# Kernel tuning notes

Measured on AMD Instinct MI355X. Metric: run time of the kernel, lower is better.

Reference implementation:

```python
import jax, jax.numpy as jnp
import numpy as np

B, S, D, H = 8, 1024, 768, 12
DH = D // H
EPS = 1e-5


def setup_inputs() -> dict:
    key = jax.random.key(0)
    ks = jax.random.split(key, 12)
    sc_h = 1.0 / np.sqrt(DH)
    sc_d = 1.0 / np.sqrt(D)
    return {
        "x": jax.random.normal(ks[0], (B, S, D), jnp.float32),
        "ln1_g": jnp.ones((D,), jnp.float32),
        "ln1_b": jnp.zeros((D,), jnp.float32),
        "Wq": jax.random.normal(ks[1], (H, DH, DH), jnp.float32) * sc_h,
        "bq": jax.random.normal(ks[2], (H, DH), jnp.float32) * 0.01,
        "Wk": jax.random.normal(ks[3], (H, DH, DH), jnp.float32) * sc_h,
        "bk": jax.random.normal(ks[4], (H, DH), jnp.float32) * 0.01,
        "Wv": jax.random.normal(ks[5], (H, DH, DH), jnp.float32) * sc_h,
        "bv": jax.random.normal(ks[6], (H, DH), jnp.float32) * 0.01,
        "ln2_g": jnp.ones((D,), jnp.float32),
        "ln2_b": jnp.zeros((D,), jnp.float32),
        "W1": jax.random.normal(ks[7], (D, 4 * D), jnp.float32) * sc_d,  # c_fc (bias=False)
        "W2": jax.random.normal(ks[8], (4 * D, D), jnp.float32) * (1.0 / np.sqrt(4 * D)),  # c_proj (bias=False)
    }


def _layernorm(x, g, b):
    m = jnp.mean(x, axis=-1, keepdims=True)
    v = jnp.mean(jnp.square(x - m), axis=-1, keepdims=True)
    return (x - m) * jax.lax.rsqrt(v + EPS) * g + b


def _msa(x, Wq, bq, Wk, bk, Wv, bv):
    b, s, d = x.shape
    h = x.reshape(b, s, H, DH)  # per-head slices of the embedding
    q = jnp.einsum('bshd,hde->bhse', h, Wq) + bq[None, :, None, :]
    k = jnp.einsum('bshd,hde->bhse', h, Wk) + bk[None, :, None, :]
    v = jnp.einsum('bshd,hde->bhse', h, Wv) + bv[None, :, None, :]
    scores = jnp.einsum('bhse,bhte->bhst', q, k) / np.sqrt(DH).astype(np.float32)
    attn = jax.nn.softmax(scores, axis=-1)
    o = jnp.einsum('bhst,bhte->bhse', attn, v)
    return o.transpose(0, 2, 1, 3).reshape(b, s, d)  # concat heads


def reference(x, ln1_g, ln1_b, Wq, bq, Wk, bk, Wv, bv, ln2_g, ln2_b, W1, W2):
    out = x + _msa(_layernorm(x, ln1_g, ln1_b), Wq, bq, Wk, bk, Wv, bv)
    h = _layernorm(out, ln2_g, ln2_b)
    ffn = jnp.dot(jax.nn.gelu(jnp.dot(h, W1), approximate=False), W2)
    return out + ffn
```

## Files before the change

kernel.cpp:

```cpp
#include <hip/hip_runtime.h>
#include <hip/hip_bf16.h>
#include <math.h>

#define B_ 8
#define S_ 1024
#define D_ 768
#define H_ 12
#define QSCALE 0.18033688011112042f

typedef __attribute__((ext_vector_type(8))) short short8;
typedef __attribute__((ext_vector_type(4))) float floatx4;
typedef unsigned short ushort_t;

__device__ __forceinline__ ushort_t f2bf(float f) {
  unsigned int u = __builtin_bit_cast(unsigned int, f);
  u += 0x7fffu + ((u >> 16) & 1u);
  return (ushort_t)(u >> 16);
}

__device__ __forceinline__ unsigned int pkbf(float a, float b) {
  __hip_bfloat162 h = __float22bfloat162_rn(make_float2(a, b));
  unsigned int r;
  __builtin_memcpy(&r, &h, sizeof(r));
  return r;
}

__device__ __forceinline__ float gelu_f(float x) {
  const float z = fabsf(x) * 0.70710678118654752f;
  const float t = __builtin_amdgcn_rcpf(1.0f + 0.3275911f * z);
  const float p =
      t * (0.254829592f +
           t * (-0.284496736f +
                t * (1.421413741f + t * (-1.453152027f + t * 1.061405429f))));
  const float e = __expf(-z * z);
  const float erfv = 1.0f - p * e;
  return 0.5f * x * (1.0f + copysignf(erfv, x));
}

template <int N>
__device__ __forceinline__ void wait_vmcnt() {
  if constexpr (N == 0)
    asm volatile("s_waitcnt vmcnt(0)" ::: "memory");
  else if constexpr (N == 3)
    asm volatile("s_waitcnt vmcnt(3)" ::: "memory");
  else if constexpr (N == 4)
    asm volatile("s_waitcnt vmcnt(4)" ::: "memory");
  else if constexpr (N == 6)
    asm volatile("s_waitcnt vmcnt(6)" ::: "memory");
  else
    asm volatile("s_waitcnt vmcnt(8)" ::: "memory");
}

__global__ __launch_bounds__(256) void ln_bf16(
    const float* __restrict__ in, const float* __restrict__ g,
    const float* __restrict__ bias, ushort_t* __restrict__ out) {
  const int row = blockIdx.x * 4 + (threadIdx.x >> 6);
  const int lane = threadIdx.x & 63;
  const float* p = in + (size_t)row * D_;
  float4 v[3];
#pragma unroll
  for (int j = 0; j < 3; ++j) v[j] = *(const float4*)(p + j * 256 + lane * 4);
  float s = 0.f;
#pragma unroll
  for (int j = 0; j < 3; ++j) s += (v[j].x + v[j].y) + (v[j].z + v[j].w);
#pragma unroll
  for (int m = 1; m < 64; m <<= 1) s += __shfl_xor(s, m);
  const float mean = s * (1.0f / D_);
  float q = 0.f;
#pragma unroll
  for (int j = 0; j < 3; ++j) {
    const float a = v[j].x - mean, b = v[j].y - mean;
    const float c = v[j].z - mean, d = v[j].w - mean;
    q += (a * a + b * b) + (c * c + d * d);
  }
#pragma unroll
  for (int m = 1; m < 64; m <<= 1) q += __shfl_xor(q, m);
  const float rstd = rsqrtf(q * (1.0f / D_) + 1e-5f);
  ushort_t* o = out + (size_t)row * D_;
#pragma unroll
  for (int j = 0; j < 3; ++j) {
    const float4 gv = *(const float4*)(g + j * 256 + lane * 4);
    const float4 bv = *(const float4*)(bias + j * 256 + lane * 4);
    const unsigned int p01 = pkbf((v[j].x - mean) * rstd * gv.x + bv.x,
                                  (v[j].y - mean) * rstd * gv.y + bv.y);
    const unsigned int p23 = pkbf((v[j].z - mean) * rstd * gv.z + bv.z,
                                  (v[j].w - mean) * rstd * gv.w + bv.w);
    *(uint2*)(o + j * 256 + lane * 4) = make_uint2(p01, p23);
  }
}

__device__ __forceinline__ void tcast_body(
    const float* __restrict__ W, ushort_t* __restrict__ Wt,
    int Kdim, int Ndim, int bx, int by, float* sh) {
  float(*tile)[33] = (float(*)[33])sh;
  const int n0 = bx * 32, k0 = by * 32;
  const int tx = threadIdx.x & 31, ty = threadIdx.x >> 5;
#pragma unroll
  for (int i = 0; i < 32; i += 8)
    tile[ty + i][tx] = W[(size_t)(k0 + ty + i) * Ndim + n0 + tx];
  __syncthreads();
#pragma unroll
  for (int i = 0; i < 32; i += 8)
    Wt[(size_t)(n0 + ty + i) * Kdim + k0 + tx] = f2bf(tile[tx][ty + i]);
}

__global__ __launch_bounds__(256) void prep_weights(
    const float* __restrict__ W1, ushort_t* __restrict__ Wt1,
    const float* __restrict__ W2, ushort_t* __restrict__ Wt2,
    const float* __restrict__ Wq, const float* __restrict__ Wk,
    const float* __restrict__ Wv, ushort_t* __restrict__ Wqt,
    ushort_t* __restrict__ Wkt, ushort_t* __restrict__ Wvt) {
  __shared__ float sh[64 * 65];
  const int bid = blockIdx.x;
  if (bid < 2304) {
    tcast_body(W1, Wt1, 768, 3072, bid % 96, bid / 96, sh);
  } else if (bid < 4608) {
    const int idx = bid - 2304;
    tcast_body(W2, Wt2, 3072, 768, idx % 24, idx / 24, sh);
  } else {
    const int idx = bid - 4608;
    const int h = idx % 12, which = idx / 12;
    const float* W = which == 0 ? Wq : which == 1 ? Wk : Wv;
    ushort_t* O = which == 0 ? Wqt : which == 1 ? Wkt : Wvt;
    float(*t)[65] = (float(*)[65])sh;
    const int tid = threadIdx.x;
#pragma unroll
    for (int i = 0; i < 16; ++i) {
      const int idx2 = tid + i * 256;
      t[idx2 >> 6][idx2 & 63] = W[h * 4096 + idx2];
    }
    __syncthreads();
#pragma unroll
    for (int i = 0; i < 16; ++i) {
      const int idx2 = tid + i * 256;
      O[h * 4096 + idx2] = f2bf(t[idx2 & 63][idx2 >> 6]);
    }
  }
}

__global__ __launch_bounds__(256) void qkv_mfma(
    const ushort_t* __restrict__ xbf,
    const ushort_t* __restrict__ Wqt, const ushort_t* __restrict__ Wkt,
    const ushort_t* __restrict__ Wvt,
    const float* __restrict__ bq, const float* __restrict__ bk,
    const float* __restrict__ bv,
    ushort_t* __restrict__ qo, ushort_t* __restrict__ ko,
    ushort_t* __restrict__ vt) {
  const int h = blockIdx.y;
  const int mb = blockIdx.x * 128;
  const int tid = threadIdx.x;
  const int wave = tid >> 6, lane = tid & 63;
  const int lc = lane & 15, kq = lane >> 4;
  const int wm = wave * 32;

  __shared__ __align__(16) ushort_t Lb[4][2560];
  ushort_t* Lw = Lb[wave];

  short8 af[2][2];
#pragma unroll
  for (int mi = 0; mi < 2; ++mi)
#pragma unroll
    for (int kc = 0; kc < 2; ++kc)
      af[mi][kc] = *(const short8*)(xbf + (size_t)(mb + wm + mi * 16 + lc) * D_ +
                                    h * 64 + kc * 32 + kq * 8);

  const ushort_t* Wp[3] = {Wqt + h * 4096, Wkt + h * 4096, Wvt + h * 4096};
  floatx4 accT[2][2][4] = {};
  floatx4 accV[2][4] = {};
#pragma unroll
  for (int n = 0; n < 4; ++n)
#pragma unroll
    for (int kc = 0; kc < 2; ++kc) {
      const short8 wq_ = *(const short8*)(Wp[0] + (n * 16 + lc) * 64 +
                                          kc * 32 + kq * 8);
      const short8 wk_ = *(const short8*)(Wp[1] + (n * 16 + lc) * 64 +
                                          kc * 32 + kq * 8);
      const short8 wv_ = *(const short8*)(Wp[2] + (n * 16 + lc) * 64 +
                                          kc * 32 + kq * 8);
#pragma unroll
      for (int mi = 0; mi < 2; ++mi) {
        accT[0][mi][n] = __builtin_amdgcn_mfma_f32_16x16x32_bf16(
            wq_, af[mi][kc], accT[0][mi][n], 0, 0, 0);
        accT[1][mi][n] = __builtin_amdgcn_mfma_f32_16x16x32_bf16(
            wk_, af[mi][kc], accT[1][mi][n], 0, 0, 0);
        accV[mi][n] = __builtin_amdgcn_mfma_f32_16x16x32_bf16(
            af[mi][kc], wv_, accV[mi][n], 0, 0, 0);
      }
    }

  const int b = mb >> 10;
  const size_t obase = (size_t)(b * H_ + h) * (S_ * 64);
  const int sbase = (mb & 1023) + wm;

#pragma unroll
  for (int w3 = 0; w3 < 2; ++w3) {
    const float* bias = (w3 == 0 ? bq : bk) + h * 64;
    ushort_t* outp = w3 == 0 ? qo : ko;
#pragma unroll
    for (int mi = 0; mi < 2; ++mi)
#pragma unroll
      for (int n = 0; n < 4; ++n) {
        const float4 bv4 = *(const float4*)(bias + n * 16 + kq * 4);
        const floatx4 v = accT[w3][mi][n];
        float v0 = v[0] + bv4.x, v1 = v[1] + bv4.y;
        float v2 = v[2] + bv4.z, v3 = v[3] + bv4.w;
        if (w3 == 0) { v0 *= QSCALE; v1 *= QSCALE; v2 *= QSCALE; v3 *= QSCALE; }
        *(uint2*)(&Lw[(mi * 16 + lc) * 72 + n * 16 + kq * 4]) =
            make_uint2(pkbf(v0, v1), pkbf(v2, v3));
      }
    asm volatile("s_waitcnt lgkmcnt(0)" ::: "memory");
    const int srow = lane >> 2, c16 = (lane & 3) * 16;
#pragma unroll
    for (int it = 0; it < 2; ++it) {
      const int s = it * 16 + srow;
      const uint4 r0 = *(const uint4*)(&Lw[s * 72 + c16]);
      const uint4 r1 = *(const uint4*)(&Lw[s * 72 + c16 + 8]);
      *(uint4*)(outp + obase + (size_t)(sbase + s) * 64 + c16) = r0;
      *(uint4*)(outp + obase + (size_t)(sbase + s) * 64 + c16 + 8) = r1;
    }
    asm volatile("s_waitcnt lgkmcnt(0)" ::: "memory");
  }

#pragma unroll
  for (int n = 0; n < 4; ++n) {
    const float bvv = bv[h * 64 + n * 16 + lc];
#pragma unroll
    for (int mi = 0; mi < 2; ++mi) {
      const floatx4 v = accV[mi][n];
      *(uint2*)(&Lw[(n * 16 + lc) * 40 + mi * 16 + kq * 4]) =
          make_uint2(pkbf(v[0] + bvv, v[1] + bvv),
                     pkbf(v[2] + bvv, v[3] + bvv));
    }
  }
  asm volatile("s_waitcnt lgkmcnt(0)" ::: "memory");
  {
    const int erow = lane >> 2, s8 = (lane & 3) * 8;
#pragma unroll
    for (int it = 0; it < 4; ++it) {
      const int e = it * 16 + erow;
      const uint4 r0 = *(const uint4*)(&Lw[e * 40 + s8]);
      *(uint4*)(vt + obase + (size_t)e * S_ + sbase + s8) = r0;
    }
  }
}

__global__ __launch_bounds__(512) void attn_mfma(
    const ushort_t* __restrict__ qb, const ushort_t* __restrict__ kb,
    const ushort_t* __restrict__ vt, const float* __restrict__ x,
    float* __restrict__ out1) {
  const int bh = blockIdx.x;
  const int tid = threadIdx.x;
  const int wave = tid >> 6, lane = tid & 63;
  const int lc = lane & 15, kq = lane >> 4;
  const int q0 = blockIdx.y * 128 + wave * 16;

  __shared__ __align__(16) ushort_t smem[8192 + 8 * 16 * 72];
  ushort_t* Ks = smem;
  ushort_t* Vs = smem + 4096;
  ushort_t* Pp = smem + 8192 + wave * (16 * 72);

  const ushort_t* qp = qb + (size_t)bh * (S_ * 64);
  const ushort_t* kp = kb + (size_t)bh * (S_ * 64);
  const ushort_t* vp = vt + (size_t)bh * (S_ * 64);

  short8 qf[2];
#pragma unroll
  for (int kc = 0; kc < 2; ++kc)
    qf[kc] = *(const short8*)(qp + (size_t)(q0 + lc) * 64 + kc * 32 + kq * 8);

  const int srow = tid >> 3;
  const int sgc = ((tid & 7) ^ (srow & 7)) * 8;
  const int slds = srow * 64 + (tid & 7) * 8;
  const int swz = lc & 7;

  float l_r = 0.0f;
  floatx4 oacc[4] = {};

  for (int kt = 0; kt < 16; ++kt) {
    __builtin_amdgcn_global_load_lds(
        (const __attribute__((address_space(1))) unsigned int*)
            (kp + (size_t)(kt * 64 + srow) * 64 + sgc),
        (__attribute__((address_space(3))) unsigned int*)(Ks + slds), 16, 0, 0);
    __builtin_amdgcn_global_load_lds(
        (const __attribute__((address_space(1))) unsigned int*)
            (vp + (size_t)srow * S_ + kt * 64 + sgc),
        (__attribute__((address_space(3))) unsigned int*)(Vs + slds), 16, 0, 0);
    __syncthreads();

    floatx4 sacc[4] = {};
#pragma unroll
    for (int mi = 0; mi < 4; ++mi) {
      const int row = (mi * 16 + lc) * 64;
#pragma unroll
      for (int kc = 0; kc < 2; ++kc) {
        const short8 kf =
            *(const short8*)(Ks + row + ((kc * 4 + kq) ^ swz) * 8);
        sacc[mi] = __builtin_amdgcn_mfma_f32_16x16x32_bf16(
            kf, qf[kc], sacc[mi], 0, 0, 0);
      }
    }

    float pr[4][4];
    float sm = 0.f;
#pragma unroll
    for (int mi = 0; mi < 4; ++mi)
#pragma unroll
      for (int r = 0; r < 4; ++r) {
        pr[mi][r] = exp2f(sacc[mi][r]);
        sm += pr[mi][r];
      }
    l_r += sm;
#pragma unroll
    for (int mi = 0; mi < 4; ++mi) {
      const unsigned int p01 = pkbf(pr[mi][0], pr[mi][1]);
      const unsigned int p23 = pkbf(pr[mi][2], pr[mi][3]);
      *(uint2*)(&Pp[lc * 72 + mi * 16 + kq * 4]) = make_uint2(p01, p23);
    }
    asm volatile("s_waitcnt lgkmcnt(0)" ::: "memory");

    short8 pf[2];
#pragma unroll
    for (int kc = 0; kc < 2; ++kc)
      pf[kc] = *(const short8*)(&Pp[lc * 72 + kc * 32 + kq * 8]);
#pragma unroll
    for (int mi = 0; mi < 4; ++mi) {
      const int row = (mi * 16 + lc) * 64;
#pragma unroll
      for (int kc = 0; kc < 2; ++kc) {
        const short8 vf =
            *(const short8*)(Vs + row + ((kc * 4 + kq) ^ swz) * 8);
        oacc[mi] = __builtin_amdgcn_mfma_f32_16x16x32_bf16(
            vf, pf[kc], oacc[mi], 0, 0, 0);
      }
    }
    __syncthreads();
  }

  const int b = bh / H_, h = bh % H_;
  float lt = l_r;
  lt += __shfl_xor(lt, 16);
  lt += __shfl_xor(lt, 32);
  const float inv = 1.0f / lt;
  float* Ow = (float*)smem + wave * 1088;
#pragma unroll
  for (int mi = 0; mi < 4; ++mi) {
    floatx4 ov = oacc[mi];
    ov[0] *= inv; ov[1] *= inv; ov[2] *= inv; ov[3] *= inv;
    *(floatx4*)(&Ow[lc * 68 + mi * 16 + kq * 4]) = ov;
  }
  asm volatile("s_waitcnt lgkmcnt(0)" ::: "memory");
  const int row = (lane >> 3) & 7, c8 = (lane & 7) * 4;
#pragma unroll
  for (int rg = 0; rg < 2; ++rg) {
    const int qq = rg * 8 + row;
    const size_t gbase =
        ((size_t)(b * S_) + q0 + qq) * D_ + h * 64 + c8;
#pragma unroll
    for (int j = 0; j < 2; ++j) {
      const float4 ov = *(const float4*)(&Ow[qq * 68 + j * 32 + c8]);
      const float4 xv = *(const float4*)(x + gbase + j * 32);
      *(float4*)(out1 + gbase + j * 32) =
          make_float4(ov.x + xv.x, ov.y + xv.y, ov.z + xv.z, ov.w + xv.w);
    }
  }
}

template <int BM, int BN, int N, int K, bool GELU, bool RESID, bool OUT_BF16,
          bool XCDMAP>
__global__ __launch_bounds__(512, 4) void gemm_pipe(
    const ushort_t* __restrict__ A, const ushort_t* __restrict__ Bt,
    const float* __restrict__ resid, void* __restrict__ Cout) {
  constexpr int MI = BM / 32;
  constexpr int NJ = BN / 64;
  constexpr int LPT = BM / 64 + BN / 64;
  constexpr int NT = K / 64;

  int mb, nb;
  if constexpr (XCDMAP) {
    const int lin = blockIdx.x;
    const int xcd = lin & 7, slot = lin >> 3;
    const int mbg = slot / (N / 128), nbi = slot - mbg * (N / 128);
    mb = (xcd * 16 + mbg) * 64;
    nb = nbi * 128;
  } else {
    nb = blockIdx.x * BN;
    mb = blockIdx.y * BM;
  }

  const int tid = threadIdx.x;
  const int wave = tid >> 6, lane = tid & 63;
  const int wm = (wave >> 2) * (BM / 2), wn = (wave & 3) * (BN / 4);

  __shared__ __align__(16) ushort_t Asp[2][BM * 64];
  __shared__ __align__(16) ushort_t Bsp[2][BN * 64];

  const int sr = tid >> 3;
  const int sc8 = (tid & 7) * 8;
  const int sgx = ((tid & 7) ^ (sr & 7)) * 8;

  auto stage = [&](int t, int buf) {
    const int kb = t * 64;
#pragma unroll
    for (int j = 0; j < BM / 64; ++j) {
      const int row = j * 64 + sr;
      __builtin_amdgcn_global_load_lds(
          (const __attribute__((address_space(1))) unsigned int*)
              (A + (size_t)(mb + row) * K + kb + sgx),
          (__attribute__((address_space(3))) unsigned int*)
              (&Asp[buf][row * 64 + sc8]), 16, 0, 0);
    }
#pragma unroll
    for (int j = 0; j < BN / 64; ++j) {
      const int row = j * 64 + sr;
      __builtin_amdgcn_global_load_lds(
          (const __attribute__((address_space(1))) unsigned int*)
              (Bt + (size_t)(nb + row) * K + kb + sgx),
          (__attribute__((address_space(3))) unsigned int*)
              (&Bsp[buf][row * 64 + sc8]), 16, 0, 0);
    }
  };

  stage(0, 0);
  stage(1, 1);
  wait_vmcnt<LPT>();
  __builtin_amdgcn_s_barrier();
  __builtin_amdgcn_sched_barrier(0);

  const int lc = lane & 15, kq = lane >> 4, swz = lc & 7;
  floatx4 acc[MI][NJ] = {};

#pragma unroll 1
  for (int t = 0; t < NT; ++t) {
    const int cur = t & 1;
    short8 af[MI][2], bfr[NJ][2];
#pragma unroll
    for (int ks = 0; ks < 2; ++ks) {
#pragma unroll
      for (int i = 0; i < MI; ++i)
        af[i][ks] = *(const short8*)(&Asp[cur][(wm + i * 16 + lc) * 64 +
                                               ((ks * 4 + kq) ^ swz) * 8]);
#pragma unroll
      for (int j = 0; j < NJ; ++j)
        bfr[j][ks] = *(const short8*)(&Bsp[cur][(wn + j * 16 + lc) * 64 +
                                                ((ks * 4 + kq) ^ swz) * 8]);
    }
    __builtin_amdgcn_s_setprio(1);
#pragma unroll
    for (int i = 0; i < MI; ++i)
#pragma unroll
      for (int j = 0; j < NJ; ++j)
        acc[i][j] = __builtin_amdgcn_mfma_f32_16x16x32_bf16(
            af[i][0], bfr[j][0], acc[i][j], 0, 0, 0);
    __builtin_amdgcn_s_setprio(0);
    asm volatile("s_waitcnt lgkmcnt(0)" ::: "memory");
    __builtin_amdgcn_sched_barrier(0);
    __builtin_amdgcn_s_barrier();
    __builtin_amdgcn_sched_barrier(0);
    if (t + 2 < NT) stage(t + 2, cur);
    __builtin_amdgcn_sched_barrier(0);
    if (t + 2 < NT)
      wait_vmcnt<LPT>();
    else if (t + 1 < NT)
      wait_vmcnt<0>();
    if (t + 1 < NT) {
      __builtin_amdgcn_s_barrier();
      __builtin_amdgcn_sched_barrier(0);
    }
    __builtin_amdgcn_s_setprio(1);
#pragma unroll
    for (int i = 0; i < MI; ++i)
#pragma unroll
      for (int j = 0; j < NJ; ++j)
        acc[i][j] = __builtin_amdgcn_mfma_f32_16x16x32_bf16(
            af[i][1], bfr[j][1], acc[i][j], 0, 0, 0);
    __builtin_amdgcn_s_setprio(0);
  }

  const int lcol = lane & 15, lr4 = (lane >> 4) * 4;
#pragma unroll
  for (int i = 0; i < MI; ++i)
#pragma unroll
    for (int r = 0; r < 4; ++r) {
      const int m = mb + wm + i * 16 + lr4 + r;
#pragma unroll
      for (int j = 0; j < NJ; ++j) {
        const int col = nb + wn + j * 16 + lcol;
        float vv = acc[i][j][r];
        if (GELU) vv = gelu_f(vv);
        if (RESID) vv += resid[(size_t)m * N + col];
        if (OUT_BF16)
          ((ushort_t*)Cout)[(size_t)m * N + col] = f2bf(vv);
        else
          ((float*)Cout)[(size_t)m * N + col] = vv;
      }
    }
}

extern "C" void kernel_launch(void* const* d_in, const int* in_sizes, int n_in,
                              void* d_out, int out_size, void* d_ws, size_t ws_size,
                              hipStream_t stream) {
  (void)in_sizes; (void)n_in; (void)out_size; (void)ws_size;
  const float* x     = (const float*)d_in[0];
  const float* ln1_g = (const float*)d_in[1];
  const float* ln1_b = (const float*)d_in[2];
  const float* Wq    = (const float*)d_in[3];
  const float* bq    = (const float*)d_in[4];
  const float* Wk    = (const float*)d_in[5];
  const float* bk    = (const float*)d_in[6];
  const float* Wv    = (const float*)d_in[7];
  const float* bv    = (const float*)d_in[8];
  const float* ln2_g = (const float*)d_in[9];
  const float* ln2_b = (const float*)d_in[10];
  const float* W1    = (const float*)d_in[11];
  const float* W2    = (const float*)d_in[12];
  float* out = (float*)d_out;

  const size_t n = (size_t)B_ * S_ * D_;
  ushort_t* u = (ushort_t*)d_ws;
  ushort_t* xbf  = u;
  ushort_t* qb   = xbf + n;
  ushort_t* kb   = qb + n;
  ushort_t* vt   = kb + n;
  ushort_t* xbf2 = vt + n;
  ushort_t* act  = xbf2 + n;
  ushort_t* Wt1  = act + (size_t)8192 * 3072;
  ushort_t* Wt2  = Wt1 + (size_t)3072 * 768;
  ushort_t* Wqt  = Wt2 + (size_t)768 * 3072;
  ushort_t* Wkt  = Wqt + H_ * 4096;
  ushort_t* Wvt  = Wkt + H_ * 4096;
  float* out1 = (float*)(Wvt + H_ * 4096);

  prep_weights<<<dim3(4644), dim3(256), 0, stream>>>(
      W1, Wt1, W2, Wt2, Wq, Wk, Wv, Wqt, Wkt, Wvt);
  ln_bf16<<<dim3(2048), dim3(256), 0, stream>>>(x, ln1_g, ln1_b, xbf);
  qkv_mfma<<<dim3(64, 12), dim3(256), 0, stream>>>(xbf, Wqt, Wkt, Wvt,
                                                   bq, bk, bv, qb, kb, vt);
  attn_mfma<<<dim3(96, 8), dim3(512), 0, stream>>>(qb, kb, vt, x, out1);
  ln_bf16<<<dim3(2048), dim3(256), 0, stream>>>(out1, ln2_g, ln2_b, xbf2);
  gemm_pipe<128, 128, 3072, 768, true, false, true, false>
      <<<dim3(24, 64), dim3(512), 0, stream>>>(xbf2, Wt1, nullptr, act);
  gemm_pipe<64, 128, 768, 3072, false, true, false, true>
      <<<dim3(768), dim3(512), 0, stream>>>(act, Wt2, out1, out);
}
```

Measured before the change: 277.7 us.

## Use triple-buffered 256x128 GEMM kernel for the GELU FC1 layer

```diff
diff --git a/kernel.cpp b/kernel.cpp
--- a/kernel.cpp
+++ b/kernel.cpp
@@ -365,6 +365,121 @@
   }
 }
 
+template <int BM, int BN, int N, int K, bool GELU, bool RESID, bool OUT_BF16>
+__global__ __launch_bounds__(512, 2) void gemm_tbuf(
+    const ushort_t* __restrict__ A, const ushort_t* __restrict__ Bt,
+    const float* __restrict__ resid, void* __restrict__ Cout) {
+  constexpr int LPTA = BM / 64;
+  constexpr int LPTB = BN / 64;
+  constexpr int LPT = LPTA + LPTB;
+  constexpr int NT = K / 64;
+  constexpr int TSZ = (BM + BN) * 64;
+
+  const int nb = blockIdx.x * BN;
+  const int mb = blockIdx.y * BM;
+  const int tid = threadIdx.x;
+  const int wave = tid >> 6, lane = tid & 63;
+  const int wm = (wave >> 1) * 64;
+  const int wn = (wave & 1) * 64;
+
+  __shared__ __align__(16) ushort_t Ls[3][TSZ];
+
+  const int sr = tid >> 3;
+  const int sc8 = (tid & 7) * 8;
+  const int sgx = ((tid & 7) ^ (sr & 7)) * 8;
+
+  auto stageAll = [&](int t, int buf) {
+    const int kb = t * 64;
+#pragma unroll
+    for (int j = 0; j < LPTA; ++j) {
+      const int row = j * 64 + sr;
+      __builtin_amdgcn_global_load_lds(
+          (const __attribute__((address_space(1))) unsigned int*)
+              (A + (size_t)(mb + row) * K + kb + sgx),
+          (__attribute__((address_space(3))) unsigned int*)
+              (&Ls[buf][row * 64 + sc8]), 16, 0, 0);
+    }
+#pragma unroll
+    for (int j = 0; j < LPTB; ++j) {
+      const int row = j * 64 + sr;
+      __builtin_amdgcn_global_load_lds(
+          (const __attribute__((address_space(1))) unsigned int*)
+              (Bt + (size_t)(nb + row) * K + kb + sgx),
+          (__attribute__((address_space(3))) unsigned int*)
+              (&Ls[buf][BM * 64 + row * 64 + sc8]), 16, 0, 0);
+    }
+  };
+
+  stageAll(0, 0);
+  stageAll(1, 1);
+  wait_vmcnt<LPT>();
+  __builtin_amdgcn_s_barrier();
+  __builtin_amdgcn_sched_barrier(0);
+
+  const int lc = lane & 15, kq = lane >> 4, swz = lc & 7;
+  floatx4 acc[4][4] = {};
+
+  int buf = 0;
+#pragma unroll 1
+  for (int t = 0; t < NT; ++t) {
+    const ushort_t* As = &Ls[buf][0];
+    const ushort_t* Bs = &Ls[buf][BM * 64];
+    int nbuf = buf + 2; if (nbuf >= 3) nbuf -= 3;
+
+    short8 af[4][2], bfr[4][2];
+#pragma unroll
+    for (int ks = 0; ks < 2; ++ks) {
+#pragma unroll
+      for (int i = 0; i < 4; ++i)
+        af[i][ks] = *(const short8*)(As + (wm + i * 16 + lc) * 64 +
+                                     ((ks * 4 + kq) ^ swz) * 8);
+#pragma unroll
+      for (int j = 0; j < 4; ++j)
+        bfr[j][ks] = *(const short8*)(Bs + (wn + j * 16 + lc) * 64 +
+                                      ((ks * 4 + kq) ^ swz) * 8);
+    }
+    if (t + 2 < NT) stageAll(t + 2, nbuf);
+    __builtin_amdgcn_s_setprio(1);
+#pragma unroll
+    for (int ks = 0; ks < 2; ++ks)
+#pragma unroll
+      for (int i = 0; i < 4; ++i)
+#pragma unroll
+        for (int j = 0; j < 4; ++j)
+          acc[i][j] = __builtin_amdgcn_mfma_f32_16x16x32_bf16(
+              af[i][ks], bfr[j][ks], acc[i][j], 0, 0, 0);
+    __builtin_amdgcn_s_setprio(0);
+    if (t + 1 < NT) {
+      if (t + 2 < NT)
+        wait_vmcnt<LPT>();
+      else
+        wait_vmcnt<0>();
+      __builtin_amdgcn_s_barrier();
+      __builtin_amdgcn_sched_barrier(0);
+    }
+    buf = (buf == 2) ? 0 : buf + 1;
+  }
+
+  const int lcol = lane & 15, lr4 = (lane >> 4) * 4;
+#pragma unroll
+  for (int i = 0; i < 4; ++i)
+#pragma unroll
+    for (int r = 0; r < 4; ++r) {
+      const int m = mb + wm + i * 16 + lr4 + r;
+#pragma unroll
+      for (int j = 0; j < 4; ++j) {
+        const int col = nb + wn + j * 16 + lcol;
+        float vv = acc[i][j][r];
+        if (GELU) vv = gelu_f(vv);
+        if (RESID) vv += resid[(size_t)m * N + col];
+        if (OUT_BF16)
+          ((ushort_t*)Cout)[(size_t)m * N + col] = f2bf(vv);
+        else
+          ((float*)Cout)[(size_t)m * N + col] = vv;
+      }
+    }
+}
+
 template <int BM, int BN, int N, int K, bool GELU, bool RESID, bool OUT_BF16,
           bool XCDMAP>
 __global__ __launch_bounds__(512, 4) void gemm_pipe(
@@ -537,8 +652,8 @@
                                                    bq, bk, bv, qb, kb, vt);
   attn_mfma<<<dim3(96, 8), dim3(512), 0, stream>>>(qb, kb, vt, x, out1);
   ln_bf16<<<dim3(2048), dim3(256), 0, stream>>>(out1, ln2_g, ln2_b, xbf2);
-  gemm_pipe<128, 128, 3072, 768, true, false, true, false>
-      <<<dim3(24, 64), dim3(512), 0, stream>>>(xbf2, Wt1, nullptr, act);
+  gemm_tbuf<256, 128, 3072, 768, true, false, true>
+      <<<dim3(24, 32), dim3(512), 0, stream>>>(xbf2, Wt1, nullptr, act);
   gemm_pipe<64, 128, 768, 3072, false, true, false, true>
       <<<dim3(768), dim3(512), 0, stream>>>(act, Wt2, out1, out);
 }
```

Result: slower. 298.8 us (+7.6%).
